# Optimization experiments

Measured on AMD Instinct MI355X. Metric: run time of the kernel, lower is better.

The kernel has to match this reference:

```python
import jax, jax.numpy as jnp
import numpy as np

N_HEAD = 16

def setup_inputs() -> dict:
    key = jax.random.key(0)
    ks = jax.random.split(key, 9)
    B, T, C = 4, 2048, 1024
    s = 0.02
    return {
        "x": jax.random.normal(ks[0], (B, T, C), dtype=jnp.float32),
        "Wq": jax.random.normal(ks[1], (C, C), dtype=jnp.float32) * s,
        "bq": jnp.zeros((C,), dtype=jnp.float32),
        "Wk": jax.random.normal(ks[2], (C, C), dtype=jnp.float32) * s,
        "bk": jnp.zeros((C,), dtype=jnp.float32),
        "Wv": jax.random.normal(ks[3], (C, C), dtype=jnp.float32) * s,
        "bv": jnp.zeros((C,), dtype=jnp.float32),
        "Wo": jax.random.normal(ks[4], (C, C), dtype=jnp.float32) * s,
        "bo": jnp.zeros((C,), dtype=jnp.float32),
    }

def reference(x, Wq, bq, Wk, bk, Wv, bv, Wo, bo):
    B, T, C = x.shape
    H = N_HEAD
    d = C // H
    # QKV projections (Linear: y = x @ W + b), split heads -> [B, H, T, d]
    def proj(W, b):
        return (x @ W + b).reshape(B, T, H, d).transpose(0, 2, 1, 3)
    q = proj(Wq, bq)
    k = proj(Wk, bk)
    v = proj(Wv, bv)
    scale = jnp.float32(d) ** -0.5
    scores = jnp.einsum("bhtd,bhsd->bhts", q, k) * scale  # [B,H,T,T]
    attn = jax.nn.softmax(scores, axis=-1)
    out = jnp.einsum("bhts,bhsd->bhtd", attn, v)  # [B,H,T,d]
    out = out.transpose(0, 2, 1, 3).reshape(B, T, C)
    return out @ Wo + bo
```

## Files before the change

kernel.cpp:

```cpp
#include <hip/hip_runtime.h>
#include <hip/hip_bf16.h>

typedef unsigned short u16;
typedef unsigned int   u32;

typedef __bf16 bf16x8 __attribute__((ext_vector_type(8)));
typedef float  f32x4  __attribute__((ext_vector_type(4)));

#define MFMA16(A, B, C) __builtin_amdgcn_mfma_f32_16x16x32_bf16(A, B, C, 0, 0, 0)

static __device__ __forceinline__ u16 f2bf(float f) {
  union { float f; u32 u; } v; v.f = f;
  u32 r = v.u + 0x7fffu + ((v.u >> 16) & 1u);
  return (u16)(r >> 16);
}

static __device__ __forceinline__ float exp2a(float x) {
  float r; asm("v_exp_f32 %0, %1" : "=v"(r) : "v"(x)); return r;
}
static __device__ __forceinline__ float max3f(float a, float b, float c) {
  float r; asm("v_max3_f32 %0, %1, %2, %3" : "=v"(r) : "v"(a), "v"(b), "v"(c)); return r;
}
static __device__ __forceinline__ u32 cvtpk(float lo, float hi) {
  u32 r; asm("v_cvt_pk_bf16_f32 %0, %1, %2" : "=v"(r) : "v"(lo), "v"(hi)); return r;
}

static __device__ __forceinline__ void async16(const void* g, void* l) {
  __builtin_amdgcn_global_load_lds((const __attribute__((address_space(1))) void*)g,
                                   (__attribute__((address_space(3))) void*)l, 16, 0, 0);
}

static __device__ __forceinline__ int permrow(int r) {
  return (r & 3) | (((r >> 3) & 1) << 2);
}

__global__ __launch_bounds__(256) void prep_k(const float* __restrict__ x, u16* __restrict__ xb,
                                              const float* __restrict__ Wq, const float* __restrict__ Wk,
                                              const float* __restrict__ Wv, const float* __restrict__ Wo,
                                              u16* __restrict__ WT) {
  __shared__ float tile[32][33];
  const int bid = blockIdx.x;
  if (bid < 8192) {
    size_t i = ((size_t)bid * 256 + threadIdx.x) * 4;
    float4 v = *(const float4*)(x + i);
    u32 lo = (u32)f2bf(v.x) | ((u32)f2bf(v.y) << 16);
    u32 hi = (u32)f2bf(v.z) | ((u32)f2bf(v.w) << 16);
    *(uint2*)(xb + i) = make_uint2(lo, hi);
  } else {
    const int rem = bid - 8192;
    const int z = rem >> 10;
    const int rr = rem & 1023;
    const int n0 = (rr & 31) * 32;
    const int k0 = (rr >> 5) * 32;
    const float* W = (z == 0) ? Wq : (z == 1) ? Wk : (z == 2) ? Wv : Wo;
    u16* out = WT + (size_t)z * 1048576;
    const int tx = threadIdx.x & 31, ty = threadIdx.x >> 5;
#pragma unroll
    for (int i = 0; i < 4; i++)
      tile[ty + i * 8][tx] = W[(size_t)(k0 + ty + i * 8) * 1024 + n0 + tx];
    __syncthreads();
#pragma unroll
    for (int i = 0; i < 4; i++)
      out[(size_t)(n0 + ty + i * 8) * 1024 + k0 + tx] = f2bf(tile[tx][ty + i * 8]);
  }
}

#define G_STAGE(NXT)                                                          \
  {                                                                           \
    async16(pgA0, &As[(NXT) * 16384 + (0 * 512 + tid) * 8]);                  \
    async16(pgA1, &As[(NXT) * 16384 + (1 * 512 + tid) * 8]);                  \
    async16(pgA2, &As[(NXT) * 16384 + (2 * 512 + tid) * 8]);                  \
    async16(pgA3, &As[(NXT) * 16384 + (3 * 512 + tid) * 8]);                  \
    async16(pgB0, &Bs[(NXT) * 8192 + (0 * 512 + tid) * 8]);                   \
    async16(pgB1, &Bs[(NXT) * 8192 + (1 * 512 + tid) * 8]);                   \
    pgA0 += 64; pgA1 += 64; pgA2 += 64; pgA3 += 64; pgB0 += 64; pgB1 += 64;   \
  }

#define COMPUTE_T(CUR)                                                        \
  _Pragma("unroll")                                                           \
  for (int kk = 0; kk < 2; ++kk) {                                            \
    const u16* pAk = kk ? pA1 : pA0;                                          \
    const u16* pBk = kk ? pB1 : pB0;                                          \
    bf16x8 a0 = *(const bf16x8*)(pAk + (CUR) * 16384);                        \
    bf16x8 a1 = *(const bf16x8*)(pAk + (CUR) * 16384 + 1024);                 \
    bf16x8 a2 = *(const bf16x8*)(pAk + (CUR) * 16384 + 2048);                 \
    bf16x8 a3 = *(const bf16x8*)(pAk + (CUR) * 16384 + 3072);                 \
    bf16x8 b0 = *(const bf16x8*)(pBk + (CUR) * 8192);                         \
    bf16x8 b1 = *(const bf16x8*)(pBk + (CUR) * 8192 + 1024);                  \
    bf16x8 b2 = *(const bf16x8*)(pBk + (CUR) * 8192 + 2048);                  \
    bf16x8 b3 = *(const bf16x8*)(pBk + (CUR) * 8192 + 3072);                  \
    __builtin_amdgcn_s_setprio(1);                                            \
    acc[0][0] = MFMA16(a0, b0, acc[0][0]); acc[0][1] = MFMA16(a0, b1, acc[0][1]); \
    acc[0][2] = MFMA16(a0, b2, acc[0][2]); acc[0][3] = MFMA16(a0, b3, acc[0][3]); \
    acc[1][0] = MFMA16(a1, b0, acc[1][0]); acc[1][1] = MFMA16(a1, b1, acc[1][1]); \
    acc[1][2] = MFMA16(a1, b2, acc[1][2]); acc[1][3] = MFMA16(a1, b3, acc[1][3]); \
    acc[2][0] = MFMA16(a2, b0, acc[2][0]); acc[2][1] = MFMA16(a2, b1, acc[2][1]); \
    acc[2][2] = MFMA16(a2, b2, acc[2][2]); acc[2][3] = MFMA16(a2, b3, acc[2][3]); \
    acc[3][0] = MFMA16(a3, b0, acc[3][0]); acc[3][1] = MFMA16(a3, b1, acc[3][1]); \
    acc[3][2] = MFMA16(a3, b2, acc[3][2]); acc[3][3] = MFMA16(a3, b3, acc[3][3]); \
    __builtin_amdgcn_s_setprio(0);                                            \
  }

#define GITER(CUR, WN, STG, NXT)                                              \
  {                                                                           \
    asm volatile("s_waitcnt vmcnt(" #WN ")" ::: "memory");                    \
    __builtin_amdgcn_s_barrier();                                             \
    __builtin_amdgcn_sched_barrier(0);                                        \
    if (STG) G_STAGE(NXT)                                                     \
    COMPUTE_T(CUR)                                                            \
  }

template <int MODE>
__global__ __launch_bounds__(512, 2) void gemm256_k(const u16* __restrict__ A, const u16* __restrict__ WTall,
                                                    const float* __restrict__ b0, const float* __restrict__ b1,
                                                    const float* __restrict__ b2,
                                                    u16* __restrict__ outb, float* __restrict__ outf) {
  __shared__ u16 As[3 * 16384];
  __shared__ u16 Bs[3 * 8192];
  const int tid = threadIdx.x;
  const int lane = tid & 63;
  const int wid = tid >> 6;
  const int wm = wid >> 1, wn = wid & 1;
  const int g = lane >> 4, cc = lane & 15;

  const int bid = blockIdx.x;
  const int xcd = bid & 7;
  const int idx = bid >> 3;
  const int m0 = (xcd * 4 + (idx & 3)) * 256;
  const int nb = (idx >> 2) * 128;
  const u16* Bg = WTall + (size_t)(MODE == 0 ? 0 : 3145728) + (size_t)nb * 1024;

  const u16* pgA0; const u16* pgA1; const u16* pgA2; const u16* pgA3;
  const u16* pgB0; const u16* pgB1;
  {
    const int u0 = tid, u1 = 512 + tid, u2 = 1024 + tid, u3 = 1536 + tid;
    pgA0 = A + (size_t)(m0 + (u0 >> 3)) * 1024 + (((u0 & 7) ^ ((u0 >> 3) & 7)) << 3);
    pgA1 = A + (size_t)(m0 + (u1 >> 3)) * 1024 + (((u1 & 7) ^ ((u1 >> 3) & 7)) << 3);
    pgA2 = A + (size_t)(m0 + (u2 >> 3)) * 1024 + (((u2 & 7) ^ ((u2 >> 3) & 7)) << 3);
    pgA3 = A + (size_t)(m0 + (u3 >> 3)) * 1024 + (((u3 & 7) ^ ((u3 >> 3) & 7)) << 3);
    pgB0 = Bg + (size_t)(u0 >> 3) * 1024 + (((u0 & 7) ^ ((u0 >> 3) & 7)) << 3);
    pgB1 = Bg + (size_t)(u1 >> 3) * 1024 + (((u1 & 7) ^ ((u1 >> 3) & 7)) << 3);
  }

  const int s0 = g ^ (cc & 7);
  const u16* pA0 = As + (wm * 64 + cc) * 64 + (s0 << 3);
  const u16* pA1 = As + (wm * 64 + cc) * 64 + ((s0 ^ 4) << 3);
  const u16* pB0 = Bs + (wn * 64 + cc) * 64 + (s0 << 3);
  const u16* pB1 = Bs + (wn * 64 + cc) * 64 + ((s0 ^ 4) << 3);

  f32x4 acc[4][4] = {};

  G_STAGE(0)
  G_STAGE(1)

  for (int to = 0; to < 12; to += 3) {
    GITER(0, 6, 1, 2)
    GITER(1, 6, 1, 0)
    GITER(2, 6, 1, 1)
  }
  GITER(0, 6, 1, 2)
  GITER(1, 6, 1, 0)
  GITER(2, 6, 0, 0)
  GITER(0, 0, 0, 0)

  const int z = (MODE == 0) ? (nb >> 10) : 0;
  const float* bias = (MODE == 0) ? (z == 0 ? b0 : (z == 1 ? b1 : b2)) : b0;
  const float scl = (MODE == 0 && z == 0) ? 0.18033688011112042f : 1.0f;

#pragma unroll
  for (int mi = 0; mi < 4; mi++) {
#pragma unroll
    for (int ni = 0; ni < 4; ni++) {
      const int ng = nb + wn * 64 + ni * 16 + cc;
      const int n = (MODE == 0) ? (ng & 1023) : ng;
      const float bn = bias[n];
      const int mb = m0 + wm * 64 + mi * 16 + g * 4;
      if (MODE == 0) {
        u16* o = outb + (size_t)z * 8388608;
        if (z == 2) {
          u16 h[4];
#pragma unroll
          for (int r = 0; r < 4; r++) h[r] = f2bf(acc[mi][ni][r] + bn);
          const size_t ix = ((size_t)(((mb >> 11) * 16 + (n >> 6)) * 64 + (n & 63))) * 2048 + (mb & 2047);
          *(uint2*)&o[ix] = make_uint2((u32)h[0] | ((u32)h[1] << 16), (u32)h[2] | ((u32)h[3] << 16));
        } else {
#pragma unroll
          for (int r = 0; r < 4; r++) {
            const int m = mb + r;
            const float val = (acc[mi][ni][r] + bn) * scl;
            o[((size_t)((m >> 11) * 16 + (n >> 6)) * 2048 + (m & 2047)) * 64 + (n & 63)] = f2bf(val);
          }
        }
      } else {
#pragma unroll
        for (int r = 0; r < 4; r++)
          outf[(size_t)(mb + r) * 1024 + n] = acc[mi][ni][r] + bn;
      }
    }
  }
}

#define SMAX(S0, S1, M, O, PF)                                                \
  {                                                                           \
    float pm_ = max3f(max3f(S0[0], S0[1], S0[2]),                             \
                      max3f(S0[3], S1[0], S1[1]), fmaxf(S1[2], S1[3]));       \
    if (__builtin_expect(!__all(pm_ <= M + 8.0f), 0)) {                       \
      pm_ = fmaxf(pm_, __shfl_xor(pm_, 16));                                  \
      pm_ = fmaxf(pm_, __shfl_xor(pm_, 32));                                  \
      const float mn_ = fmaxf(M, pm_);                                        \
      const float al_ = exp2a(M - mn_);                                       \
      _Pragma("unroll")                                                       \
      for (int r_ = 0; r_ < 4; ++r_) {                                        \
        const float ar_ = __shfl(al_, g * 4 + r_);                            \
        _Pragma("unroll")                                                     \
        for (int t_ = 0; t_ < 5; ++t_) O[t_][r_] *= ar_;                      \
      }                                                                       \
      M = mn_;                                                                \
    }                                                                         \
    const float e0_ = exp2a(S0[0] - M), e1_ = exp2a(S0[1] - M);               \
    const float e2_ = exp2a(S0[2] - M), e3_ = exp2a(S0[3] - M);               \
    const float e4_ = exp2a(S1[0] - M), e5_ = exp2a(S1[1] - M);               \
    const float e6_ = exp2a(S1[2] - M), e7_ = exp2a(S1[3] - M);               \
    union { u32 u[4]; bf16x8 v; } pu_;                                        \
    pu_.u[0] = cvtpk(e0_, e1_); pu_.u[1] = cvtpk(e2_, e3_);                   \
    pu_.u[2] = cvtpk(e4_, e5_); pu_.u[3] = cvtpk(e6_, e7_);                   \
    PF = pu_.v;                                                               \
  }

#define COMPUTE(BUF)                                                          \
  _Pragma("unroll")                                                           \
  for (int sub = 0; sub < 2; ++sub) {                                         \
    const u16* pV_ = sub ? pV1 : pV0;                                         \
    bf16x8 k00 = *(const bf16x8*)(pK0 + (BUF)*4096 + sub*2048);               \
    bf16x8 k01 = *(const bf16x8*)(pK1 + (BUF)*4096 + sub*2048);               \
    bf16x8 k10 = *(const bf16x8*)(pK0 + (BUF)*4096 + sub*2048 + 256);         \
    bf16x8 k11 = *(const bf16x8*)(pK1 + (BUF)*4096 + sub*2048 + 256);         \
    __builtin_amdgcn_s_setprio(1);                                            \
    f32x4 sA0 = {}, sA1 = {}, sB0 = {}, sB1 = {};                             \
    sA0 = MFMA16(k00, qfA[0], sA0); sA0 = MFMA16(k01, qfA[1], sA0);           \
    sB0 = MFMA16(k00, qfB[0], sB0); sB0 = MFMA16(k01, qfB[1], sB0);           \
    sA1 = MFMA16(k10, qfA[0], sA1); sA1 = MFMA16(k11, qfA[1], sA1);           \
    sB1 = MFMA16(k10, qfB[0], sB1); sB1 = MFMA16(k11, qfB[1], sB1);           \
    __builtin_amdgcn_s_setprio(0);                                            \
    bf16x8 pfA, pfB;                                                          \
    SMAX(sA0, sA1, mA, oA, pfA);                                              \
    SMAX(sB0, sB1, mB, oB, pfB);                                              \
    __builtin_amdgcn_s_setprio(1);                                            \
    _Pragma("unroll")                                                         \
    for (int t = 0; t < 4; ++t) {                                             \
      bf16x8 vf = *(const bf16x8*)(pV_ + (BUF)*4096 + t*1024);                \
      oA[t] = MFMA16(pfA, vf, oA[t]);                                         \
      oB[t] = MFMA16(pfB, vf, oB[t]);                                         \
    }                                                                         \
    oA[4] = MFMA16(pfA, vone, oA[4]);                                         \
    oB[4] = MFMA16(pfB, vone, oB[4]);                                         \
    __builtin_amdgcn_s_setprio(0);                                            \
  }

#define STEP(BUF, IT)                                                         \
  {                                                                           \
    __syncthreads();                                                          \
    if ((IT) < 31) {                                                          \
      const size_t ko_ = (size_t)((IT) + 1) * 4096;                           \
      const size_t vo_ = (size_t)((IT) + 1) * 64;                             \
      async16(kS0 + ko_, &Ks[((BUF) ^ 1) * 4096 + tid * 8]);                  \
      async16(kS1 + ko_, &Ks[((BUF) ^ 1) * 4096 + tid * 8 + 2048]);           \
      async16(vS0 + vo_, &Vs[((BUF) ^ 1) * 4096 + tid * 8]);                  \
      async16(vS1 + vo_, &Vs[((BUF) ^ 1) * 4096 + tid * 8 + 2048]);           \
    }                                                                         \
    COMPUTE(BUF)                                                              \
  }

__global__ __launch_bounds__(256, 4) void attn_k(const u16* __restrict__ Qg, const u16* __restrict__ Kg,
                                                 const u16* __restrict__ Vtg, u16* __restrict__ ctx) {
  __shared__ u16 Ks[8192];
  __shared__ u16 Vs[8192];
  const int tid = threadIdx.x;
  const int lane = tid & 63;
  const int wid = tid >> 6;
  const int g = lane >> 4, cc = lane & 15;
  const int a_ = cc >> 2, b_ = cc & 3;

  const int bid = blockIdx.x;
  const int xcd = bid & 7, tt = bid >> 3;
  const int bh = xcd * 8 + (tt >> 4);
  const int q0 = (tt & 15) * 128 + wid * 16;
  const size_t base = (size_t)bh * 131072;

  bf16x8 qfA[2], qfB[2];
#pragma unroll
  for (int c2 = 0; c2 < 2; c2++) {
    qfA[c2] = *(const bf16x8*)(Qg + base + (size_t)(q0 + cc) * 64 + c2 * 32 + g * 8);
    qfB[c2] = *(const bf16x8*)(Qg + base + (size_t)(q0 + 64 + cc) * 64 + c2 * 32 + g * 8);
  }

  bf16x8 vone;
#pragma unroll
  for (int j = 0; j < 8; j++) vone[j] = (__bf16)1.0f;

  float mA = -30000.0f, mB = -30000.0f;
  f32x4 oA[5] = {}, oB[5] = {};

  const int cK = b_ | ((a_ & 1) << 2);
  const int slK = g ^ cK;
  const u16* pK0 = &Ks[(8 * a_ + b_) * 64 + (slK << 3)];
  const u16* pK1 = &Ks[(8 * a_ + b_) * 64 + ((slK ^ 4) << 3)];
  const int cV = b_ | (((cc >> 3) & 1) << 2);
  const u16* pV0 = &Vs[cc * 64 + ((g ^ cV) << 3)];
  const u16* pV1 = &Vs[cc * 64 + (((4 + g) ^ cV) << 3)];

  const int r0 = tid >> 3, r1 = r0 + 32;
  const int slot = tid & 7;
  const int sp0 = slot ^ permrow(r0), sp1 = slot ^ permrow(r1);
  const u16* kS0 = Kg + base + (size_t)r0 * 64 + (sp0 << 3);
  const u16* kS1 = Kg + base + (size_t)r1 * 64 + (sp1 << 3);
  const u16* vS0 = Vtg + base + (size_t)r0 * 2048 + (sp0 << 3);
  const u16* vS1 = Vtg + base + (size_t)r1 * 2048 + (sp1 << 3);

  async16(kS0, &Ks[tid * 8]);
  async16(kS1, &Ks[tid * 8 + 2048]);
  async16(vS0, &Vs[tid * 8]);
  async16(vS1, &Vs[tid * 8 + 2048]);

  for (int it = 0; it < 32; it += 2) {
    STEP(0, it)
    STEP(1, it + 1)
  }

  const int b = bh >> 4, h = bh & 15;
#pragma unroll
  for (int r = 0; r < 4; r++) {
    {
      const float inv = __builtin_amdgcn_rcpf(oA[4][r]);
      const int q = q0 + g * 4 + r;
#pragma unroll
      for (int t = 0; t < 4; t++)
        ctx[((size_t)((b * 2048 + q) * 16 + h)) * 64 + t * 16 + cc] = f2bf(oA[t][r] * inv);
    }
    {
      const float inv = __builtin_amdgcn_rcpf(oB[4][r]);
      const int q = q0 + 64 + g * 4 + r;
#pragma unroll
      for (int t = 0; t < 4; t++)
        ctx[((size_t)((b * 2048 + q) * 16 + h)) * 64 + t * 16 + cc] = f2bf(oB[t][r] * inv);
    }
  }
}

extern "C" void kernel_launch(void* const* d_in, const int* in_sizes, int n_in,
                              void* d_out, int out_size, void* d_ws, size_t ws_size,
                              hipStream_t stream) {
  const float* x  = (const float*)d_in[0];
  const float* Wq = (const float*)d_in[1];
  const float* bq = (const float*)d_in[2];
  const float* Wk = (const float*)d_in[3];
  const float* bk = (const float*)d_in[4];
  const float* Wv = (const float*)d_in[5];
  const float* bv = (const float*)d_in[6];
  const float* Wo = (const float*)d_in[7];
  const float* bo = (const float*)d_in[8];
  float* out = (float*)d_out;

  char* w = (char*)d_ws;
  u16* xb   = (u16*)(w);
  u16* WT   = (u16*)(w + (16u << 20));
  u16* QKV  = (u16*)(w + (24u << 20));
  u16* ctxb = (u16*)(w + (72u << 20));

  prep_k<<<dim3(12288), dim3(256), 0, stream>>>(x, xb, Wq, Wk, Wv, Wo, WT);
  gemm256_k<0><<<dim3(768), dim3(512), 0, stream>>>(xb, WT, bq, bk, bv, QKV, nullptr);
  attn_k<<<dim3(1024), dim3(256), 0, stream>>>(QKV, QKV + 8388608, QKV + 2 * 8388608, ctxb);
  gemm256_k<1><<<dim3(256), dim3(512), 0, stream>>>(ctxb, WT, bo, nullptr, nullptr, nullptr, out);
}
```

Measured before the change: 177.0 us.

## Triple-buffer K tiles and prefetch K two iterations ahead with explicit vmcnt waits

Replaces the double-buffered K/V pipeline with a three-stage K ring buffer and double-buffered V. K is prefetched two tiles ahead and V one tile ahead. __syncthreads is replaced with an explicit s_waitcnt vmcnt plus s_barrier so outstanding loads can stay in flight across iterations. This aims to hide global load latency better, at the cost of more LDS per block (which may affect occupancy at 4 blocks/CU) and a fully unrolled schedule.

Result: no change. 176.2 us (median of 2 runs) (-0.4%).

```diff
diff --git a/kernel.cpp b/kernel.cpp
--- a/kernel.cpp
+++ b/kernel.cpp
@@ -227,14 +227,14 @@
     PF = pu_.v;                                                               \
   }
 
-#define COMPUTE(BUF)                                                          \
+#define COMPUTE(KB, VB)                                                       \
   _Pragma("unroll")                                                           \
   for (int sub = 0; sub < 2; ++sub) {                                         \
     const u16* pV_ = sub ? pV1 : pV0;                                         \
-    bf16x8 k00 = *(const bf16x8*)(pK0 + (BUF)*4096 + sub*2048);               \
-    bf16x8 k01 = *(const bf16x8*)(pK1 + (BUF)*4096 + sub*2048);               \
-    bf16x8 k10 = *(const bf16x8*)(pK0 + (BUF)*4096 + sub*2048 + 256);         \
-    bf16x8 k11 = *(const bf16x8*)(pK1 + (BUF)*4096 + sub*2048 + 256);         \
+    bf16x8 k00 = *(const bf16x8*)(pK0 + (KB)*4096 + sub*2048);                \
+    bf16x8 k01 = *(const bf16x8*)(pK1 + (KB)*4096 + sub*2048);                \
+    bf16x8 k10 = *(const bf16x8*)(pK0 + (KB)*4096 + sub*2048 + 256);          \
+    bf16x8 k11 = *(const bf16x8*)(pK1 + (KB)*4096 + sub*2048 + 256);          \
     __builtin_amdgcn_s_setprio(1);                                            \
     f32x4 sA0 = {}, sA1 = {}, sB0 = {}, sB1 = {};                             \
     sA0 = MFMA16(k00, qfA[0], sA0); sA0 = MFMA16(k01, qfA[1], sA0);           \
@@ -248,7 +248,7 @@
     __builtin_amdgcn_s_setprio(1);                                            \
     _Pragma("unroll")                                                         \
     for (int t = 0; t < 4; ++t) {                                             \
-      bf16x8 vf = *(const bf16x8*)(pV_ + (BUF)*4096 + t*1024);                \
+      bf16x8 vf = *(const bf16x8*)(pV_ + (VB)*4096 + t*1024);                 \
       oA[t] = MFMA16(pfA, vf, oA[t]);                                         \
       oB[t] = MFMA16(pfB, vf, oB[t]);                                         \
     }                                                                         \
@@ -257,24 +257,28 @@
     __builtin_amdgcn_s_setprio(0);                                            \
   }
 
-#define STEP(BUF, IT)                                                         \
+#define ASTEP(KB, VB, IT, WN, SK, SV, KSB, VSB)                               \
   {                                                                           \
-    __syncthreads();                                                          \
-    if ((IT) < 31) {                                                          \
-      const size_t ko_ = (size_t)((IT) + 1) * 4096;                           \
+    asm volatile("s_waitcnt vmcnt(" #WN ")" ::: "memory");                    \
+    __builtin_amdgcn_s_barrier();                                             \
+    __builtin_amdgcn_sched_barrier(0);                                        \
+    if (SV) {                                                                 \
       const size_t vo_ = (size_t)((IT) + 1) * 64;                             \
-      async16(kS0 + ko_, &Ks[((BUF) ^ 1) * 4096 + tid * 8]);                  \
-      async16(kS1 + ko_, &Ks[((BUF) ^ 1) * 4096 + tid * 8 + 2048]);           \
-      async16(vS0 + vo_, &Vs[((BUF) ^ 1) * 4096 + tid * 8]);                  \
-      async16(vS1 + vo_, &Vs[((BUF) ^ 1) * 4096 + tid * 8 + 2048]);           \
+      async16(vS0 + vo_, &Vs[(VSB) * 4096 + tid * 8]);                        \
+      async16(vS1 + vo_, &Vs[(VSB) * 4096 + tid * 8 + 2048]);                 \
     }                                                                         \
-    COMPUTE(BUF)                                                              \
+    if (SK) {                                                                 \
+      const size_t ko_ = (size_t)((IT) + 2) * 4096;                           \
+      async16(kS0 + ko_, &Ks[(KSB) * 4096 + tid * 8]);                        \
+      async16(kS1 + ko_, &Ks[(KSB) * 4096 + tid * 8 + 2048]);                 \
+    }                                                                         \
+    COMPUTE(KB, VB)                                                           \
   }
 
 __global__ __launch_bounds__(256, 4) void attn_k(const u16* __restrict__ Qg, const u16* __restrict__ Kg,
                                                  const u16* __restrict__ Vtg, u16* __restrict__ ctx) {
-  __shared__ u16 Ks[8192];
-  __shared__ u16 Vs[8192];
+  __shared__ u16 Ks[3 * 4096];
+  __shared__ u16 Vs[2 * 4096];
   const int tid = threadIdx.x;
   const int lane = tid & 63;
   const int wid = tid >> 6;
@@ -321,11 +325,27 @@
   async16(kS1, &Ks[tid * 8 + 2048]);
   async16(vS0, &Vs[tid * 8]);
   async16(vS1, &Vs[tid * 8 + 2048]);
-
-  for (int it = 0; it < 32; it += 2) {
-    STEP(0, it)
-    STEP(1, it + 1)
-  }
+  async16(kS0 + 4096, &Ks[4096 + tid * 8]);
+  async16(kS1 + 4096, &Ks[4096 + tid * 8 + 2048]);
+  async16(vS0 + 64, &Vs[4096 + tid * 8]);
+  async16(vS1 + 64, &Vs[4096 + tid * 8 + 2048]);
+
+  ASTEP(0, 0, 0, 4, 1, 0, 2, 0)
+  for (int itb = 1; itb <= 19; itb += 6) {
+    ASTEP(1, 1, itb + 0, 2, 1, 1, 0, 0)
+    ASTEP(2, 0, itb + 1, 2, 1, 1, 1, 1)
+    ASTEP(0, 1, itb + 2, 2, 1, 1, 2, 0)
+    ASTEP(1, 0, itb + 3, 2, 1, 1, 0, 1)
+    ASTEP(2, 1, itb + 4, 2, 1, 1, 1, 0)
+    ASTEP(0, 0, itb + 5, 2, 1, 1, 2, 1)
+  }
+  ASTEP(1, 1, 25, 2, 1, 1, 0, 0)
+  ASTEP(2, 0, 26, 2, 1, 1, 1, 1)
+  ASTEP(0, 1, 27, 2, 1, 1, 2, 0)
+  ASTEP(1, 0, 28, 2, 1, 1, 0, 1)
+  ASTEP(2, 1, 29, 2, 1, 1, 1, 0)
+  ASTEP(0, 0, 30, 2, 0, 1, 0, 1)
+  ASTEP(1, 1, 31, 0, 0, 0, 0, 0)
 
   const int b = bh >> 4, h = bh & 15;
 #pragma unroll
```
